# Kernel tuning notes

Measured on AMD Instinct MI355X. Metric: run time of the kernel, lower is better.

The kernel has to match this reference:

```python
import jax, jax.numpy as jnp
import numpy as np

MASK_VALUE = -10000.0  # module uses masked_fill(-10000), not -inf


def setup_inputs() -> dict:
    key = jax.random.key(0)
    kq, kk, kv = jax.random.split(key, 3)
    B, H, S, D = 2, 16, 2048, 64
    return {
        "query_states": jax.random.normal(kq, (B, H, S, D), dtype=jnp.float32),
        "key_states": jax.random.normal(kk, (B, H, S, D), dtype=jnp.float32),
        "value_states": jax.random.normal(kv, (B, H, S, D), dtype=jnp.float32),
    }


def reference(query_states, key_states, value_states):
    B, H, S, D = query_states.shape
    kv_len = key_states.shape[-2]
    scale = 1.0 / jnp.sqrt(jnp.asarray(D, dtype=query_states.dtype))
    # [B,H,S,kv] scores
    scores = jnp.einsum("bhqd,bhkd->bhqk", query_states, key_states) * scale
    # causal mask: positions strictly above the diagonal are masked (triu diag=1)
    causal = jnp.arange(kv_len)[None, :] > jnp.arange(S)[:, None]  # [S, kv]
    scores = jnp.where(causal[None, None], MASK_VALUE, scores)
    # softmax in float32 (module upcasts), then back to input dtype
    probs = jax.nn.softmax(scores.astype(jnp.float32), axis=-1).astype(query_states.dtype)
    return jnp.einsum("bhqk,bhkd->bhqd", probs, value_states)
```

## Files before the change

### kernel.cpp

```cpp
#include <hip/hip_runtime.h>


#define S_LEN 2048
#define D_DIM 64
#define QSCALE 0.1803368867f
#define CSHIFT 23.0831206542f
#define BHSTR 131072

typedef __attribute__((ext_vector_type(8))) short short8;
typedef __attribute__((ext_vector_type(4))) short short4v;
typedef __attribute__((ext_vector_type(4))) float float4v;

typedef const __attribute__((address_space(1))) void cg_void;
typedef __attribute__((address_space(3))) void lds_void;

__device__ __forceinline__ short f2bf(float x) {
    union { float f; unsigned u; } c; c.f = x;
    unsigned u = c.u + 0x7fffu + ((c.u >> 16) & 1u);
    return (short)(u >> 16);
}

#if __has_builtin(__builtin_amdgcn_mfma_f32_16x16x16_bf16)
__device__ __forceinline__ float4v mfma16(short4v a, short4v b, float4v c) {
    return __builtin_amdgcn_mfma_f32_16x16x16_bf16(a, b, c, 0, 0, 0);
}
#elif __has_builtin(__builtin_amdgcn_mfma_f32_16x16x16bf16_1k)
__device__ __forceinline__ float4v mfma16(short4v a, short4v b, float4v c) {
    return __builtin_amdgcn_mfma_f32_16x16x16bf16_1k(a, b, c, 0, 0, 0);
}
#else
__device__ __forceinline__ float4v mfma16(short4v a, short4v b, float4v c) {
    float4v d;
    asm("v_mfma_f32_16x16x16_bf16 %0, %1, %2, %3"
        : "=v"(d) : "v"(a), "v"(b), "0"(c));
    return d;
}
#endif

#define PVS 80
__global__ __launch_bounds__(256, 4)
void prep(const float* __restrict__ K, const float* __restrict__ V,
          short* __restrict__ Kbf, short* __restrict__ Vt) {
    __shared__ __align__(16) short Vl[D_DIM * PVS];
    const int tid = threadIdx.x;
    const int st  = blockIdx.x;
    const int bh  = blockIdx.y;
    const size_t base = ((size_t)bh * S_LEN + st * 64) * D_DIM;

    #pragma unroll
    for (int i = 0; i < 4; ++i) {
        const int e = (i * 256 + tid) * 4;
        const int kv = e >> 6, d0 = e & 63;
        float4v k4 = *(const float4v*)(K + base + e);
        short4v ks = { f2bf(k4.x), f2bf(k4.y), f2bf(k4.z), f2bf(k4.w) };
        *(short4v*)(Kbf + base + e) = ks;
        float4v v4 = *(const float4v*)(V + base + e);
        Vl[(d0 + 0) * PVS + kv] = f2bf(v4.x);
        Vl[(d0 + 1) * PVS + kv] = f2bf(v4.y);
        Vl[(d0 + 2) * PVS + kv] = f2bf(v4.z);
        Vl[(d0 + 3) * PVS + kv] = f2bf(v4.w);
    }
    __syncthreads();
    const int d = tid >> 2, c = tid & 3;
    short8 a = *(const short8*)&Vl[d * PVS + c * 16];
    short8 b = *(const short8*)&Vl[d * PVS + c * 16 + 8];
    short* dst = Vt + (size_t)bh * BHSTR + (size_t)d * S_LEN + st * 64 + c * 16;
    *(short8*)dst = a;
    *(short8*)(dst + 8) = b;
}

__global__ __launch_bounds__(128, 2)
void fa_fwd5(const float* __restrict__ Q, const short* __restrict__ Kbf,
             const short* __restrict__ Vt, float* __restrict__ O) {
    __shared__ __align__(16) short SB[9216];

    const int tid  = threadIdx.x;
    const int w    = tid >> 6;
    const int lane = tid & 63;
    const int l15  = lane & 15;
    const int quad = lane >> 4;

    const int bh  = blockIdx.y;
    const int blk = gridDim.x - 1 - blockIdx.x;
    const int q0  = blk * 64;

    const float* Qb  = Q + (size_t)bh * S_LEN * D_DIM;
    const short* KbB = Kbf + (size_t)bh * BHSTR;
    const short* VtB = Vt  + (size_t)bh * BHSTR;
    float*       Ob  = O + (size_t)bh * S_LEN * D_DIM;

    const short* gsrc[9]; int gcoef[9];
    #pragma unroll
    for (int i = 0; i < 9; ++i) {
        const int s = i * 128 + tid;
        if (s < 576) {
            const int row = s / 9, j = s - row * 9;
            const int j8 = (j == 8) ? 0 : j;
            gsrc[i] = KbB + row * 64 + j8 * 8;
            gcoef[i] = 4096;
        } else {
            const int ss = s - 576;
            const int row = ss / 9, j = ss - row * 9;
            const int j8 = (j == 8) ? 7 : j;
            gsrc[i] = VtB + (size_t)row * S_LEN + j8 * 8;
            gcoef[i] = 64;
        }
    }

    short8 qfrag[2][2];
    #pragma unroll
    for (int qt = 0; qt < 2; ++qt) {
        const float* qp = Qb + (size_t)(q0 + (w * 2 + qt) * 16 + l15) * D_DIM;
        #pragma unroll
        for (int c = 0; c < 2; ++c) {
            const int d0 = c * 32 + quad * 8;
            float4v a = *(const float4v*)(qp + d0);
            float4v b = *(const float4v*)(qp + d0 + 4);
            qfrag[qt][c][0] = f2bf(a.x * QSCALE); qfrag[qt][c][1] = f2bf(a.y * QSCALE);
            qfrag[qt][c][2] = f2bf(a.z * QSCALE); qfrag[qt][c][3] = f2bf(a.w * QSCALE);
            qfrag[qt][c][4] = f2bf(b.x * QSCALE); qfrag[qt][c][5] = f2bf(b.y * QSCALE);
            qfrag[qt][c][6] = f2bf(b.z * QSCALE); qfrag[qt][c][7] = f2bf(b.w * QSCALE);
        }
    }

    float l_lane[2] = {0.f, 0.f};
    float4v o_acc[2][4];
    #pragma unroll
    for (int qt = 0; qt < 2; ++qt)
        #pragma unroll
        for (int td = 0; td < 4; ++td) o_acc[qt][td] = (float4v)0.0f;

    const short* Ks = SB;
    const short* Vs = SB + 4608;
    const int n_tiles = blk + 1;

    for (int t = 0; t < n_tiles; ++t) {
        __syncthreads();
        #pragma unroll
        for (int i = 0; i < 9; ++i)
            __builtin_amdgcn_global_load_lds(
                (cg_void*)(gsrc[i] + (size_t)t * gcoef[i]),
                (lds_void*)&SB[i * 1024 + w * 512],
                16, 0, 0);
        __syncthreads();

        float4v sc[2][4];
        #pragma unroll
        for (int tt = 0; tt < 4; ++tt) {
            const short* kr = &Ks[(tt * 16 + l15) * 72 + quad * 8];
            short8 k0 = *(const short8*)(kr);
            short8 k1 = *(const short8*)(kr + 32);
            #pragma unroll
            for (int qt = 0; qt < 2; ++qt) {
                float4v acc = (float4v)0.0f;
                acc = __builtin_amdgcn_mfma_f32_16x16x32_bf16(k0, qfrag[qt][0], acc, 0, 0, 0);
                acc = __builtin_amdgcn_mfma_f32_16x16x32_bf16(k1, qfrag[qt][1], acc, 0, 0, 0);
                sc[qt][tt] = acc;
            }
        }

        if (t == blk) {
            #pragma unroll
            for (int qt = 0; qt < 2; ++qt) {
                const int qrow = q0 + (w * 2 + qt) * 16 + l15;
                #pragma unroll
                for (int tt = 0; tt < 4; ++tt) {
                    const int kv = t * 64 + tt * 16 + quad * 4;
                    #pragma unroll
                    for (int r = 0; r < 4; ++r)
                        if (kv + r > qrow) sc[qt][tt][r] = -3.0e38f;
                }
            }
        }

        short4v pb[2][4];
        #pragma unroll
        for (int qt = 0; qt < 2; ++qt)
            #pragma unroll
            for (int tt = 0; tt < 4; ++tt) {
                #pragma unroll
                for (int r = 0; r < 4; ++r) {
                    float p = __builtin_amdgcn_exp2f(sc[qt][tt][r] - CSHIFT);
                    sc[qt][tt][r] = p;
                    l_lane[qt] += p;
                }
                pb[qt][tt] = short4v{ f2bf(sc[qt][tt][0]), f2bf(sc[qt][tt][1]),
                                      f2bf(sc[qt][tt][2]), f2bf(sc[qt][tt][3]) };
            }

        #pragma unroll
        for (int td = 0; td < 4; ++td) {
            const short* vr = &Vs[(td * 16 + l15) * 72 + quad * 4];
            #pragma unroll
            for (int tt = 0; tt < 4; ++tt) {
                short4v va = *(const short4v*)(vr + tt * 16);
                #pragma unroll
                for (int qt = 0; qt < 2; ++qt)
                    o_acc[qt][td] = mfma16(va, pb[qt][tt], o_acc[qt][td]);
            }
        }
    }

    #pragma unroll
    for (int qt = 0; qt < 2; ++qt) {
        float l = l_lane[qt];
        l += __shfl_xor(l, 16);
        l += __shfl_xor(l, 32);
        const float inv = 1.0f / l;
        const int qrow = q0 + (w * 2 + qt) * 16 + l15;
        float* op = Ob + (size_t)qrow * D_DIM + quad * 4;
        #pragma unroll
        for (int td = 0; td < 4; ++td) {
            float4v st = { o_acc[qt][td][0] * inv, o_acc[qt][td][1] * inv,
                           o_acc[qt][td][2] * inv, o_acc[qt][td][3] * inv };
            *(float4v*)(op + td * 16) = st;
        }
    }
}

#define KSTR 72
__global__ __launch_bounds__(256, 2)
void fa_fwd_fb(const float* __restrict__ Q, const float* __restrict__ K,
               const float* __restrict__ V, float* __restrict__ O) {
    __shared__ __align__(16) short Ksf[64 * KSTR];
    __shared__ __align__(16) short Vsf[D_DIM * KSTR];
    __shared__ __align__(16) short Psf[4 * 16 * KSTR];

    const int tid = threadIdx.x, w = tid >> 6, lane = tid & 63;
    const int l15 = lane & 15, quad = lane >> 4;
    const int bh = blockIdx.y, blk = gridDim.x - 1 - blockIdx.x, q0 = blk * 64;
    const float* Qb = Q + (size_t)bh * S_LEN * D_DIM;
    const float* Kb = K + (size_t)bh * S_LEN * D_DIM;
    const float* Vb = V + (size_t)bh * S_LEN * D_DIM;
    float* Ob = O + (size_t)bh * S_LEN * D_DIM;

    short8 qfrag[2];
    {
        const float* qp = Qb + (size_t)(q0 + w * 16 + l15) * D_DIM;
        #pragma unroll
        for (int c = 0; c < 2; ++c) {
            const int d0 = c * 32 + quad * 8;
            float4v a = *(const float4v*)(qp + d0);
            float4v b = *(const float4v*)(qp + d0 + 4);
            qfrag[c][0] = f2bf(a.x * 0.125f); qfrag[c][1] = f2bf(a.y * 0.125f);
            qfrag[c][2] = f2bf(a.z * 0.125f); qfrag[c][3] = f2bf(a.w * 0.125f);
            qfrag[c][4] = f2bf(b.x * 0.125f); qfrag[c][5] = f2bf(b.y * 0.125f);
            qfrag[c][6] = f2bf(b.z * 0.125f); qfrag[c][7] = f2bf(b.w * 0.125f);
        }
    }
    const int crow0 = q0 + w * 16 + quad * 4;
    float m_run[4], l_run[4];
    float4v o_acc[4];
    #pragma unroll
    for (int r = 0; r < 4; ++r) { m_run[r] = -1e30f; l_run[r] = 0.0f; }
    #pragma unroll
    for (int td = 0; td < 4; ++td) o_acc[td] = (float4v)0.0f;
    short* Pw = Psf + w * 16 * KSTR;
    const int n_tiles = blk + 1;

    for (int t = 0; t < n_tiles; ++t) {
        const int kv0 = t * 64;
        __syncthreads();
        #pragma unroll
        for (int i = 0; i < 4; ++i) {
            const int slot = tid + i * 256;
            const int row = slot >> 4, d4 = (slot & 15) << 2;
            float4v k4 = *(const float4v*)(Kb + (size_t)(kv0 + row) * D_DIM + d4);
            short4v ks = { f2bf(k4.x), f2bf(k4.y), f2bf(k4.z), f2bf(k4.w) };
            *(short4v*)&Ksf[row * KSTR + d4] = ks;
            float4v v4 = *(const float4v*)(Vb + (size_t)(kv0 + row) * D_DIM + d4);
            Vsf[(d4 + 0) * KSTR + row] = f2bf(v4.x);
            Vsf[(d4 + 1) * KSTR + row] = f2bf(v4.y);
            Vsf[(d4 + 2) * KSTR + row] = f2bf(v4.z);
            Vsf[(d4 + 3) * KSTR + row] = f2bf(v4.w);
        }
        __syncthreads();
        float4v sc[4];
        #pragma unroll
        for (int tt = 0; tt < 4; ++tt) {
            float4v acc = (float4v)0.0f;
            #pragma unroll
            for (int c = 0; c < 2; ++c) {
                short8 bf = *(const short8*)&Ksf[(tt * 16 + l15) * KSTR + c * 32 + quad * 8];
                acc = __builtin_amdgcn_mfma_f32_16x16x32_bf16(qfrag[c], bf, acc, 0, 0, 0);
            }
            sc[tt] = acc;
        }
        if (t == n_tiles - 1) {
            #pragma unroll
            for (int tt = 0; tt < 4; ++tt) {
                const int col = kv0 + tt * 16 + l15;
                #pragma unroll
                for (int r = 0; r < 4; ++r)
                    if (col > crow0 + r) sc[tt][r] = -1e30f;
            }
        }
        #pragma unroll
        for (int r = 0; r < 4; ++r) {
            float mx = fmaxf(fmaxf(sc[0][r], sc[1][r]), fmaxf(sc[2][r], sc[3][r]));
            #pragma unroll
            for (int off = 1; off <= 8; off <<= 1)
                mx = fmaxf(mx, __shfl_xor(mx, off));
            const float m_new = fmaxf(m_run[r], mx);
            const float alpha = __expf(m_run[r] - m_new);
            m_run[r] = m_new;
            float rs = 0.0f;
            #pragma unroll
            for (int tt = 0; tt < 4; ++tt) {
                float pv = __expf(sc[tt][r] - m_new);
                sc[tt][r] = pv; rs += pv;
            }
            #pragma unroll
            for (int off = 1; off <= 8; off <<= 1)
                rs += __shfl_xor(rs, off);
            l_run[r] = l_run[r] * alpha + rs;
            #pragma unroll
            for (int td = 0; td < 4; ++td) o_acc[td][r] *= alpha;
        }
        #pragma unroll
        for (int tt = 0; tt < 4; ++tt)
            #pragma unroll
            for (int r = 0; r < 4; ++r)
                Pw[(quad * 4 + r) * KSTR + tt * 16 + l15] = f2bf(sc[tt][r]);
        short8 pf[2];
        #pragma unroll
        for (int c = 0; c < 2; ++c)
            pf[c] = *(const short8*)&Pw[l15 * KSTR + c * 32 + quad * 8];
        #pragma unroll
        for (int td = 0; td < 4; ++td)
            #pragma unroll
            for (int c = 0; c < 2; ++c) {
                short8 bv = *(const short8*)&Vsf[(td * 16 + l15) * KSTR + c * 32 + quad * 8];
                o_acc[td] = __builtin_amdgcn_mfma_f32_16x16x32_bf16(pf[c], bv, o_acc[td], 0, 0, 0);
            }
    }
    #pragma unroll
    for (int td = 0; td < 4; ++td)
        #pragma unroll
        for (int r = 0; r < 4; ++r)
            Ob[(size_t)(crow0 + r) * D_DIM + td * 16 + l15] = o_acc[td][r] / l_run[r];
}

extern "C" void kernel_launch(void* const* d_in, const int* in_sizes, int n_in,
                              void* d_out, int out_size, void* d_ws, size_t ws_size,
                              hipStream_t stream) {
    const float* Q = (const float*)d_in[0];
    const float* K = (const float*)d_in[1];
    const float* V = (const float*)d_in[2];
    float* O = (float*)d_out;
    const size_t elems = (size_t)2 * 16 * S_LEN * D_DIM;
    if (ws_size >= 2 * elems * sizeof(short)) {
        short* Kbf = (short*)d_ws;
        short* Vt  = Kbf + elems;
        prep<<<dim3(32, 32), 256, 0, stream>>>(K, V, Kbf, Vt);
        fa_fwd5<<<dim3(32, 32), 128, 0, stream>>>(Q, Kbf, Vt, O);
    } else {
        fa_fwd_fb<<<dim3(32, 32), 256, 0, stream>>>(Q, K, V, O);
    }
}
```

Baseline: 147.0 us.

## Load two KV tiles per barrier, XOR-swizzle LDS, and remap block schedule

The attention loop now stages two 64-key K/V tiles into LDS per barrier pair, which halves the number of synchronisations per block. LDS padding (stride 72) is replaced by an XOR swizzle on 16-byte chunks to avoid bank conflicts in a denser layout. The grid becomes 1D with a mapping that interleaves heads and alternates forward and reverse causal tile order, to balance work across CUs. LDS per block grows to 32KB, which may lower occupancy, and odd tile counts load one unused tile.

```diff
diff --git a/kernel.cpp b/kernel.cpp
--- a/kernel.cpp
+++ b/kernel.cpp
@@ -70,9 +70,9 @@
 }
 
 __global__ __launch_bounds__(128, 2)
-void fa_fwd5(const float* __restrict__ Q, const short* __restrict__ Kbf,
-             const short* __restrict__ Vt, float* __restrict__ O) {
-    __shared__ __align__(16) short SB[9216];
+void fa_fwd12(const float* __restrict__ Q, const short* __restrict__ Kbf,
+              const short* __restrict__ Vt, float* __restrict__ O) {
+    __shared__ __align__(16) short SB[16384];
 
     const int tid  = threadIdx.x;
     const int w    = tid >> 6;
@@ -80,29 +80,37 @@
     const int l15  = lane & 15;
     const int quad = lane >> 4;
 
-    const int bh  = blockIdx.y;
-    const int blk = gridDim.x - 1 - blockIdx.x;
-    const int q0  = blk * 64;
+    const int g   = blockIdx.x;
+    const int x   = g & 7;
+    const int j   = g >> 3;
+    const int bhl = j >> 5;
+    const int c   = j & 31;
+    int T;
+    if      (bhl == 0) T = c;
+    else if (bhl == 1) T = 31 - c;
+    else if (bhl == 2) T = (c + 16) & 31;
+    else               T = 31 - ((c + 16) & 31);
+    const int bh  = x + 8 * bhl;
+    const int blk = T;
+    const int q0  = T * 64;
 
     const float* Qb  = Q + (size_t)bh * S_LEN * D_DIM;
     const short* KbB = Kbf + (size_t)bh * BHSTR;
     const short* VtB = Vt  + (size_t)bh * BHSTR;
     float*       Ob  = O + (size_t)bh * S_LEN * D_DIM;
 
-    const short* gsrc[9]; int gcoef[9];
-    #pragma unroll
-    for (int i = 0; i < 9; ++i) {
+    const short* gsrc[8]; int gcoef[8];
+    #pragma unroll
+    for (int i = 0; i < 8; ++i) {
         const int s = i * 128 + tid;
-        if (s < 576) {
-            const int row = s / 9, j = s - row * 9;
-            const int j8 = (j == 8) ? 0 : j;
-            gsrc[i] = KbB + row * 64 + j8 * 8;
+        if (s < 512) {
+            const int row = s >> 3, jj = (s ^ (s >> 3)) & 7;
+            gsrc[i] = KbB + row * 64 + jj * 8;
             gcoef[i] = 4096;
         } else {
-            const int ss = s - 576;
-            const int row = ss / 9, j = ss - row * 9;
-            const int j8 = (j == 8) ? 7 : j;
-            gsrc[i] = VtB + (size_t)row * S_LEN + j8 * 8;
+            const int sv = s - 512;
+            const int d = sv >> 3, jj = (sv ^ (sv >> 3)) & 7;
+            gsrc[i] = VtB + (size_t)d * S_LEN + jj * 8;
             gcoef[i] = 64;
         }
     }
@@ -112,14 +120,14 @@
     for (int qt = 0; qt < 2; ++qt) {
         const float* qp = Qb + (size_t)(q0 + (w * 2 + qt) * 16 + l15) * D_DIM;
         #pragma unroll
-        for (int c = 0; c < 2; ++c) {
-            const int d0 = c * 32 + quad * 8;
+        for (int cc = 0; cc < 2; ++cc) {
+            const int d0 = cc * 32 + quad * 8;
             float4v a = *(const float4v*)(qp + d0);
             float4v b = *(const float4v*)(qp + d0 + 4);
-            qfrag[qt][c][0] = f2bf(a.x * QSCALE); qfrag[qt][c][1] = f2bf(a.y * QSCALE);
-            qfrag[qt][c][2] = f2bf(a.z * QSCALE); qfrag[qt][c][3] = f2bf(a.w * QSCALE);
-            qfrag[qt][c][4] = f2bf(b.x * QSCALE); qfrag[qt][c][5] = f2bf(b.y * QSCALE);
-            qfrag[qt][c][6] = f2bf(b.z * QSCALE); qfrag[qt][c][7] = f2bf(b.w * QSCALE);
+            qfrag[qt][cc][0] = f2bf(a.x * QSCALE); qfrag[qt][cc][1] = f2bf(a.y * QSCALE);
+            qfrag[qt][cc][2] = f2bf(a.z * QSCALE); qfrag[qt][cc][3] = f2bf(a.w * QSCALE);
+            qfrag[qt][cc][4] = f2bf(b.x * QSCALE); qfrag[qt][cc][5] = f2bf(b.y * QSCALE);
+            qfrag[qt][cc][6] = f2bf(b.z * QSCALE); qfrag[qt][cc][7] = f2bf(b.w * QSCALE);
         }
     }
 
@@ -130,73 +138,89 @@
         #pragma unroll
         for (int td = 0; td < 4; ++td) o_acc[qt][td] = (float4v)0.0f;
 
-    const short* Ks = SB;
-    const short* Vs = SB + 4608;
-    const int n_tiles = blk + 1;
-
-    for (int t = 0; t < n_tiles; ++t) {
+    const int nch = (blk + 2) >> 1;
+
+    for (int ch = 0; ch < nch; ++ch) {
+        const int t0 = ch * 2;
         __syncthreads();
         #pragma unroll
-        for (int i = 0; i < 9; ++i)
+        for (int i = 0; i < 8; ++i) {
             __builtin_amdgcn_global_load_lds(
-                (cg_void*)(gsrc[i] + (size_t)t * gcoef[i]),
-                (lds_void*)&SB[i * 1024 + w * 512],
-                16, 0, 0);
+                (cg_void*)(gsrc[i] + (size_t)t0 * gcoef[i]),
+                (lds_void*)&SB[i * 1024 + w * 512], 16, 0, 0);
+            __builtin_amdgcn_global_load_lds(
+                (cg_void*)(gsrc[i] + (size_t)(t0 + 1) * gcoef[i]),
+                (lds_void*)&SB[8192 + i * 1024 + w * 512], 16, 0, 0);
+        }
         __syncthreads();
 
-        float4v sc[2][4];
-        #pragma unroll
-        for (int tt = 0; tt < 4; ++tt) {
-            const short* kr = &Ks[(tt * 16 + l15) * 72 + quad * 8];
-            short8 k0 = *(const short8*)(kr);
-            short8 k1 = *(const short8*)(kr + 32);
-            #pragma unroll
-            for (int qt = 0; qt < 2; ++qt) {
-                float4v acc = (float4v)0.0f;
-                acc = __builtin_amdgcn_mfma_f32_16x16x32_bf16(k0, qfrag[qt][0], acc, 0, 0, 0);
-                acc = __builtin_amdgcn_mfma_f32_16x16x32_bf16(k1, qfrag[qt][1], acc, 0, 0, 0);
-                sc[qt][tt] = acc;
-            }
-        }
-
-        if (t == blk) {
-            #pragma unroll
-            for (int qt = 0; qt < 2; ++qt) {
-                const int qrow = q0 + (w * 2 + qt) * 16 + l15;
+        #pragma unroll
+        for (int p = 0; p < 2; ++p) {
+            const int t = t0 + p;
+            if (t <= blk) {
+                const short* Ks = SB + p * 8192;
+                const short* Vs = Ks + 4096;
+
+                float4v sc[2][4];
                 #pragma unroll
                 for (int tt = 0; tt < 4; ++tt) {
-                    const int kv = t * 64 + tt * 16 + quad * 4;
+                    const int row = tt * 16 + l15;
+                    const int rb  = row & 7;
+                    const short* krow = Ks + row * 64;
+                    short8 k0 = *(const short8*)(krow + ((quad ^ rb) << 3));
+                    short8 k1 = *(const short8*)(krow + ((quad ^ rb ^ 4) << 3));
                     #pragma unroll
-                    for (int r = 0; r < 4; ++r)
-                        if (kv + r > qrow) sc[qt][tt][r] = -3.0e38f;
+                    for (int qt = 0; qt < 2; ++qt) {
+                        float4v acc = (float4v)0.0f;
+                        acc = __builtin_amdgcn_mfma_f32_16x16x32_bf16(k0, qfrag[qt][0], acc, 0, 0, 0);
+                        acc = __builtin_amdgcn_mfma_f32_16x16x32_bf16(k1, qfrag[qt][1], acc, 0, 0, 0);
+                        sc[qt][tt] = acc;
+                    }
                 }
-            }
-        }
-
-        short4v pb[2][4];
-        #pragma unroll
-        for (int qt = 0; qt < 2; ++qt)
-            #pragma unroll
-            for (int tt = 0; tt < 4; ++tt) {
-                #pragma unroll
-                for (int r = 0; r < 4; ++r) {
-                    float p = __builtin_amdgcn_exp2f(sc[qt][tt][r] - CSHIFT);
-                    sc[qt][tt][r] = p;
-                    l_lane[qt] += p;
+
+                if (t == blk) {
+                    #pragma unroll
+                    for (int qt = 0; qt < 2; ++qt) {
+                        const int qrow = q0 + (w * 2 + qt) * 16 + l15;
+                        #pragma unroll
+                        for (int tt = 0; tt < 4; ++tt) {
+                            const int kv = t * 64 + tt * 16 + quad * 4;
+                            #pragma unroll
+                            for (int r = 0; r < 4; ++r)
+                                if (kv + r > qrow) sc[qt][tt][r] = -3.0e38f;
+                        }
+                    }
                 }
-                pb[qt][tt] = short4v{ f2bf(sc[qt][tt][0]), f2bf(sc[qt][tt][1]),
-                                      f2bf(sc[qt][tt][2]), f2bf(sc[qt][tt][3]) };
-            }
-
-        #pragma unroll
-        for (int td = 0; td < 4; ++td) {
-            const short* vr = &Vs[(td * 16 + l15) * 72 + quad * 4];
-            #pragma unroll
-            for (int tt = 0; tt < 4; ++tt) {
-                short4v va = *(const short4v*)(vr + tt * 16);
+
+                short4v pb[2][4];
                 #pragma unroll
                 for (int qt = 0; qt < 2; ++qt)
-                    o_acc[qt][td] = mfma16(va, pb[qt][tt], o_acc[qt][td]);
+                    #pragma unroll
+                    for (int tt = 0; tt < 4; ++tt) {
+                        #pragma unroll
+                        for (int r = 0; r < 4; ++r) {
+                            float pv = __builtin_amdgcn_exp2f(sc[qt][tt][r] - CSHIFT);
+                            sc[qt][tt][r] = pv;
+                            l_lane[qt] += pv;
+                        }
+                        pb[qt][tt] = short4v{ f2bf(sc[qt][tt][0]), f2bf(sc[qt][tt][1]),
+                                              f2bf(sc[qt][tt][2]), f2bf(sc[qt][tt][3]) };
+                    }
+
+                #pragma unroll
+                for (int td = 0; td < 4; ++td) {
+                    const int d  = td * 16 + l15;
+                    const int db = d & 7;
+                    const short* vrow = Vs + d * 64 + ((quad & 1) << 2);
+                    #pragma unroll
+                    for (int tt = 0; tt < 4; ++tt) {
+                        const int jv = tt * 2 + (quad >> 1);
+                        short4v va = *(const short4v*)(vrow + ((jv ^ db) << 3));
+                        #pragma unroll
+                        for (int qt = 0; qt < 2; ++qt)
+                            o_acc[qt][td] = mfma16(va, pb[qt][tt], o_acc[qt][td]);
+                    }
+                }
             }
         }
     }
@@ -353,7 +377,7 @@
         short* Kbf = (short*)d_ws;
         short* Vt  = Kbf + elems;
         prep<<<dim3(32, 32), 256, 0, stream>>>(K, V, Kbf, Vt);
-        fa_fwd5<<<dim3(32, 32), 128, 0, stream>>>(Q, Kbf, Vt, O);
+        fa_fwd12<<<dim3(1024, 1), 128, 0, stream>>>(Q, Kbf, Vt, O);
     } else {
         fa_fwd_fb<<<dim3(32, 32), 256, 0, stream>>>(Q, K, V, O);
     }
```

Result: faster. 137.4 us (-6.5%).
